# Kernel tuning notes

Hardware: AMD Instinct MI355X
Metric: run time of the kernel (lower is better)

## Reference

```python
import jax, jax.numpy as jnp
import numpy as np

B, C, H, W, NH = 8, 512, 32, 32, 8
HD = C // NH
SCALE = HD ** -0.5


def reshape_for_attention(t, num_heads):
    # faithful to torch: view(B,nh,hd,HW) -> permute(0,3,1,2) -> view(B*nh, HW, hd)
    b, c, h, w = t.shape
    t = t.reshape(b, num_heads, c // num_heads, h * w)
    t = jnp.transpose(t, (0, 3, 1, 2))  # [B, HW, nh, hd]
    return t.reshape(b * num_heads, h * w, c // num_heads)


def reshape_from_attention(t, original_shape, num_heads):
    b, c, h, w = original_shape
    t = t.reshape(b, h * w, num_heads, c // num_heads)
    t = jnp.transpose(t, (0, 2, 3, 1))  # [B, nh, hd, HW]
    return t.reshape(b, c, h, w)


def setup_inputs() -> dict:
    key = jax.random.key(0)
    ks = jax.random.split(key, 6)
    s = (2.0 / C) ** 0.5  # kaiming-ish scale for 1x1 convs
    return {
        "x": jax.random.normal(ks[0], (B, C, H, W), dtype=jnp.float32),
        "wq": jax.random.normal(ks[1], (C, C), dtype=jnp.float32) * s,
        "wk": jax.random.normal(ks[2], (C, C), dtype=jnp.float32) * s,
        "wv": jax.random.normal(ks[3], (C, C), dtype=jnp.float32) * s,
        "wo": jax.random.normal(ks[4], (C, C), dtype=jnp.float32) * s,
        "ln_gamma": jnp.ones((C,), dtype=jnp.float32),
        "ln_beta": jnp.zeros((C,), dtype=jnp.float32),
        "gamma": jnp.zeros((1,), dtype=jnp.float32),
    }


def reference(x, wq, wk, wv, wo, ln_gamma, ln_beta, gamma):
    b, c, h, w = x.shape
    residual = x
    # 1x1 convs, no bias == channel GEMMs
    q = jnp.einsum('oc,bchw->bohw', wq, x)
    k = jnp.einsum('oc,bchw->bohw', wk, x)
    v = jnp.einsum('oc,bchw->bohw', wv, x)
    q = reshape_for_attention(q, NH)  # [B*nh, N, hd]
    k = reshape_for_attention(k, NH)
    v = reshape_for_attention(v, NH)
    attn = jnp.einsum('bnd,bmd->bnm', q, k) * SCALE  # [B*nh, N, N]
    attn = jax.nn.softmax(attn, axis=-1)
    attn_out = jnp.einsum('bnm,bmd->bnd', attn, v)
    attn_out = reshape_from_attention(attn_out, (b, c, h, w), NH)
    out = jnp.einsum('oc,bchw->bohw', wo, attn_out)
    # post-LN over channel dim
    out = jnp.transpose(out, (0, 2, 3, 1))  # [B,H,W,C]
    mu = jnp.mean(out, axis=-1, keepdims=True)
    var = jnp.var(out, axis=-1, keepdims=True)
    out = (out - mu) * jax.lax.rsqrt(var + 1e-5) * ln_gamma + ln_beta
    out = jnp.transpose(out, (0, 3, 1, 2))  # [B,C,H,W]
    return gamma * out + residual
```

## Files before the change

kernel.cpp:

```cpp
#include <hip/hip_runtime.h>
#include <hip/hip_bf16.h>


#define B_  8
#define C_  512
#define N_  1024
#define NH_ 8
#define HD_ 64

typedef __bf16 bf16x8 __attribute__((ext_vector_type(8)));
typedef __bf16 bf16x4 __attribute__((ext_vector_type(4)));
typedef float  f32x4  __attribute__((ext_vector_type(4)));

#define MFMA16(a, b, c) __builtin_amdgcn_mfma_f32_16x16x32_bf16((a), (b), (c), 0, 0, 0)

__device__ __forceinline__ void gload16(const void* g, void* l) {
    __builtin_amdgcn_global_load_lds(
        (const __attribute__((address_space(1))) unsigned int*)g,
        (__attribute__((address_space(3))) unsigned int*)l, 16, 0, 0);
}

__global__ __launch_bounds__(256) void k_prep(const float* __restrict__ x,
                                              const float* __restrict__ wq,
                                              const float* __restrict__ wk,
                                              const float* __restrict__ wv,
                                              const float* __restrict__ wo,
                                              __bf16* __restrict__ xt,
                                              __bf16* __restrict__ wcat) {
    __shared__ float tile[64][68];
    int blk = blockIdx.x;
    int tid = threadIdx.x;
    if (blk < 1024) {
        int b   = blk >> 7;
        int rem = blk & 127;
        int ct  = rem >> 4;
        int pt  = rem & 15;
        int c0 = ct * 64, p0 = pt * 64;
        for (int i = 0; i < 4; ++i) {
            int vi = i * 256 + tid;
            int c = vi >> 4, p4 = (vi & 15) * 4;
            f32x4 v = *(const f32x4*)(x + ((size_t)(b * C_ + c0 + c)) * N_ + p0 + p4);
            *(f32x4*)&tile[c][p4] = v;
        }
        __syncthreads();
        for (int i = 0; i < 4; ++i) {
            int vi = i * 256 + tid;
            int p = vi >> 4, c4 = (vi & 15) * 4;
            bf16x4 v;
            for (int j = 0; j < 4; ++j) v[j] = (__bf16)tile[c4 + j][p];
            *(bf16x4*)(xt + ((size_t)(b * N_ + p0 + p)) * C_ + c0 + c4) = v;
        }
    } else {
        int idx = (blk - 1024) * 256 + tid;
        int mat = idx >> 16;
        int off = (idx & 65535) * 4;
        const float* w = (mat == 0) ? wq : (mat == 1) ? wk : (mat == 2) ? wv : wo;
        f32x4 v = *(const f32x4*)(w + off);
        bf16x4 o;
        for (int j = 0; j < 4; ++j) o[j] = (__bf16)v[j];
        *(bf16x4*)(wcat + (size_t)mat * 262144 + off) = o;
    }
}

__global__ __launch_bounds__(256) void k_qkv(const __bf16* __restrict__ xt,
                                             const __bf16* __restrict__ wcat,
                                             __bf16* __restrict__ qa,
                                             __bf16* __restrict__ ka,
                                             __bf16* __restrict__ vt) {
    int blk  = blockIdx.x;
    int mat  = blk >> 8;
    int rem  = blk & 255;
    int b    = rem >> 5;
    int tile = rem & 31;
    int tid = threadIdx.x, lane = tid & 63, wid = tid >> 6;
    int quad = lane >> 4, l16 = lane & 15;

    const __bf16* w = wcat + (size_t)mat * 262144;
    const __bf16 *A, *Bm;
    int am0, bn0;
    if (mat < 2) {
        int mt = tile >> 2, nt = tile & 3;
        A   = xt + (size_t)b * N_ * C_;  am0 = mt * 128 + (wid >> 1) * 64;
        Bm  = w;                         bn0 = nt * 128 + (wid & 1) * 64;
    } else {
        int mt = tile & 3, nt = tile >> 2;
        A   = w;                         am0 = mt * 128 + (wid >> 1) * 64;
        Bm  = xt + (size_t)b * N_ * C_;  bn0 = nt * 128 + (wid & 1) * 64;
    }

    f32x4 acc[4][4] = {};
    for (int ks = 0; ks < 16; ++ks) {
        int kc = ks * 32 + quad * 8;
        bf16x8 af[4], bfr[4];
        for (int i = 0; i < 4; ++i)
            af[i] = *(const bf16x8*)(A + (size_t)(am0 + i * 16 + l16) * C_ + kc);
        for (int i = 0; i < 4; ++i)
            bfr[i] = *(const bf16x8*)(Bm + (size_t)(bn0 + i * 16 + l16) * C_ + kc);
        for (int mi = 0; mi < 4; ++mi)
            for (int ni = 0; ni < 4; ++ni)
                acc[mi][ni] = MFMA16(af[mi], bfr[ni], acc[mi][ni]);
    }

    if (mat < 2) {
        __bf16* dst = (mat == 0) ? qa : ka;
        for (int mi = 0; mi < 4; ++mi)
            for (int r = 0; r < 4; ++r) {
                int p = am0 + mi * 16 + quad * 4 + r;
                int g = b * NH_ + (p >> 7);
                int nbase = (p & 127) * 8;
                for (int ni = 0; ni < 4; ++ni) {
                    int o = bn0 + ni * 16 + l16;
                    dst[((size_t)g * N_ + nbase + (o >> 6)) * HD_ + (o & 63)] =
                        (__bf16)acc[mi][ni][r];
                }
            }
    } else {
        for (int mi = 0; mi < 4; ++mi)
            for (int r = 0; r < 4; ++r) {
                int o = am0 + mi * 16 + quad * 4 + r;
                int m = o & 63, i = o >> 6;
                for (int ni = 0; ni < 4; ++ni) {
                    int p = bn0 + ni * 16 + l16;
                    int g = b * NH_ + (p >> 7);
                    vt[((size_t)g * HD_ + m) * N_ + (p & 127) * 8 + i] =
                        (__bf16)acc[mi][ni][r];
                }
            }
    }
}

__global__ __launch_bounds__(256) void k_attn(const __bf16* __restrict__ qa,
                                              const __bf16* __restrict__ ka,
                                              const __bf16* __restrict__ vt,
                                              __bf16* __restrict__ ap) {
    __shared__ __bf16 Kb[2][4096];
    __shared__ __bf16 Vb[2][4096];
    __shared__ __bf16 plds[4][32][64];
    int blk = blockIdx.x;
    int g  = ((blk & 7) << 3) | ((blk >> 3) & 7);
    int qb = blk >> 6;
    int tid = threadIdx.x, lane = tid & 63, wid = tid >> 6;
    int quad = lane >> 4, l16 = lane & 15;
    int q0 = qb * 128 + wid * 32;

    const __bf16* qp = qa + (size_t)g * N_ * HD_;
    const char* kbb = (const char*)(ka + (size_t)g * N_ * HD_);
    const char* vbb = (const char*)(vt + (size_t)g * HD_ * N_);

    bf16x8 qA0 = *(const bf16x8*)(qp + (size_t)(q0 + l16) * HD_ + quad * 8);
    bf16x8 qA1 = *(const bf16x8*)(qp + (size_t)(q0 + l16) * HD_ + 32 + quad * 8);
    bf16x8 qB0 = *(const bf16x8*)(qp + (size_t)(q0 + 16 + l16) * HD_ + quad * 8);
    bf16x8 qB1 = *(const bf16x8*)(qp + (size_t)(q0 + 16 + l16) * HD_ + 32 + quad * 8);

    int lrow = lane >> 3;
    int scol = ((lane & 7) * 16) ^ (lrow << 4);
    const char* kSrc = kbb + (size_t)(wid * 16 + lrow) * 128  + scol;
    const char* vSrc = vbb + (size_t)(wid * 16 + lrow) * 2048 + scol;
    char* kds[2] = {(char*)&Kb[0][0] + wid * 2048, (char*)&Kb[1][0] + wid * 2048};
    char* vds[2] = {(char*)&Vb[0][0] + wid * 2048, (char*)&Vb[1][0] + wid * 2048};

    gload16(kSrc,          kds[0]);
    gload16(kSrc + 1024,   kds[0] + 1024);
    gload16(vSrc,          vds[0]);
    gload16(vSrc + 16384,  vds[0] + 1024);
    asm volatile("s_waitcnt vmcnt(0)" ::: "memory");
    __syncthreads();

    float liA = 0.f, liB = 0.f;
    f32x4 oA[4] = {}, oB[4] = {};
    const float sc = 0.125f * 1.44269504088896340736f;
    const int swzP = (l16 & 7) * 8;
    const int fsw  = (l16 & 7) << 4;

    int cur = 0;
    for (int t = 0; t < 16; ++t) {
        int jn = ((t + 1) & 15) * 64;
        gload16(kSrc + (size_t)jn * 128,          kds[cur ^ 1]);
        gload16(kSrc + (size_t)jn * 128 + 1024,   kds[cur ^ 1] + 1024);
        gload16(vSrc + jn * 2,                    vds[cur ^ 1]);
        gload16(vSrc + jn * 2 + 16384,            vds[cur ^ 1] + 1024);

        const char* kt = (const char*)&Kb[cur][0] - (size_t)0;
        kt = (const char*)&Kb[cur][0];
        bf16x8 kc0[4], kc1[4];
        for (int tt = 0; tt < 4; ++tt) {
            int rb = (tt * 16 + l16) * 128;
            kc0[tt] = *(const bf16x8*)(kt + rb + ((quad * 16) ^ fsw));
            kc1[tt] = *(const bf16x8*)(kt + rb + ((64 + quad * 16) ^ fsw));
        }
        f32x4 sA[4] = {}, sB[4] = {};
        for (int tt = 0; tt < 4; ++tt) {
            sA[tt] = MFMA16(kc0[tt], qA0, sA[tt]);
            sA[tt] = MFMA16(kc1[tt], qA1, sA[tt]);
            sB[tt] = MFMA16(kc0[tt], qB0, sB[tt]);
            sB[tt] = MFMA16(kc1[tt], qB1, sB[tt]);
        }

        for (int tt = 0; tt < 4; ++tt) {
            bf16x4 pkA, pkB;
            for (int r = 0; r < 4; ++r) {
                float pvA = exp2f(sA[tt][r] * sc);
                float pvB = exp2f(sB[tt][r] * sc);
                liA += pvA; liB += pvB;
                pkA[r] = (__bf16)pvA; pkB[r] = (__bf16)pvB;
            }
            int ks = (tt * 16 + quad * 4) ^ swzP;
            *(bf16x4*)&plds[wid][l16][ks]      = pkA;
            *(bf16x4*)&plds[wid][16 + l16][ks] = pkB;
        }

        asm volatile("" ::: "memory");
        const char* vtl = (const char*)&Vb[cur][0];
        for (int h = 0; h < 2; ++h) {
            int ks = (h * 32 + quad * 8) ^ swzP;
            bf16x8 pA = *(const bf16x8*)&plds[wid][l16][ks];
            bf16x8 pB = *(const bf16x8*)&plds[wid][16 + l16][ks];
            for (int dd = 0; dd < 4; ++dd) {
                bf16x8 av = *(const bf16x8*)(vtl + (dd * 16 + l16) * 128
                                             + ((h * 64 + quad * 16) ^ fsw));
                oA[dd] = MFMA16(av, pA, oA[dd]);
                oB[dd] = MFMA16(av, pB, oB[dd]);
            }
        }
        asm volatile("" ::: "memory");

        asm volatile("s_waitcnt vmcnt(0)" ::: "memory");
        __syncthreads();
        cur ^= 1;
    }

    liA += __shfl_xor(liA, 16, 64); liA += __shfl_xor(liA, 32, 64);
    liB += __shfl_xor(liB, 16, 64); liB += __shfl_xor(liB, 32, 64);

    int b = g >> 3, hi = g & 7;
    float invA = 1.0f / liA, invB = 1.0f / liB;
    int nA = q0 + l16, nB = q0 + 16 + l16;
    __bf16* dA = ap + ((size_t)(b * N_ + hi * 128 + (nA >> 3))) * C_ + (nA & 7) * 64;
    __bf16* dB = ap + ((size_t)(b * N_ + hi * 128 + (nB >> 3))) * C_ + (nB & 7) * 64;
    for (int dd = 0; dd < 4; ++dd) {
        bf16x4 oa, ob;
        for (int r = 0; r < 4; ++r) {
            oa[r] = (__bf16)(oA[dd][r] * invA);
            ob[r] = (__bf16)(oB[dd][r] * invB);
        }
        *(bf16x4*)(dA + dd * 16 + quad * 4) = oa;
        *(bf16x4*)(dB + dd * 16 + quad * 4) = ob;
    }
}

__global__ __launch_bounds__(256) void k_oproj(const __bf16* __restrict__ apm,
                                               const __bf16* __restrict__ wob,
                                               __bf16* __restrict__ o0) {
    int blk = blockIdx.x;
    int b = blk >> 5, tile = blk & 31;
    int mt = tile >> 2, nt = tile & 3;
    int tid = threadIdx.x, lane = tid & 63, wid = tid >> 6;
    int quad = lane >> 4, l16 = lane & 15;
    int am0 = mt * 128 + (wid >> 1) * 64;
    int bn0 = nt * 128 + (wid & 1) * 64;
    const __bf16* A = apm + (size_t)b * N_ * C_;

    f32x4 acc[4][4] = {};
    for (int ks = 0; ks < 16; ++ks) {
        int kc = ks * 32 + quad * 8;
        bf16x8 af[4], bfr[4];
        for (int i = 0; i < 4; ++i)
            af[i] = *(const bf16x8*)(A + (size_t)(am0 + i * 16 + l16) * C_ + kc);
        for (int i = 0; i < 4; ++i)
            bfr[i] = *(const bf16x8*)(wob + (size_t)(bn0 + i * 16 + l16) * C_ + kc);
        for (int mi = 0; mi < 4; ++mi)
            for (int ni = 0; ni < 4; ++ni)
                acc[mi][ni] = MFMA16(af[mi], bfr[ni], acc[mi][ni]);
    }
    for (int mi = 0; mi < 4; ++mi)
        for (int r = 0; r < 4; ++r) {
            int p = am0 + mi * 16 + quad * 4 + r;
            __bf16* dst = o0 + ((size_t)(b * N_ + p)) * C_;
            for (int ni = 0; ni < 4; ++ni)
                dst[bn0 + ni * 16 + l16] = (__bf16)acc[mi][ni][r];
        }
}

__global__ __launch_bounds__(256) void k_ln(const __bf16* __restrict__ o0,
                                            const float* __restrict__ x,
                                            const float* __restrict__ lng,
                                            const float* __restrict__ lnb,
                                            const float* __restrict__ gm,
                                            float* __restrict__ out) {
    __shared__ __bf16 tile[32][C_ + 4];
    int blk = blockIdx.x;
    int b = blk >> 5, pt = blk & 31;
    int p0 = pt * 32;
    int tid = threadIdx.x, lane = tid & 63, wid = tid >> 6;
    float g = gm[0];
    float lg[8], lb[8];
    *(f32x4*)&lg[0] = *(const f32x4*)(lng + lane * 8);
    *(f32x4*)&lg[4] = *(const f32x4*)(lng + lane * 8 + 4);
    *(f32x4*)&lb[0] = *(const f32x4*)(lnb + lane * 8);
    *(f32x4*)&lb[4] = *(const f32x4*)(lnb + lane * 8 + 4);

    for (int i = 0; i < 8; ++i) {
        int p = wid * 8 + i;
        bf16x8 v = *(const bf16x8*)(o0 + ((size_t)(b * N_ + p0 + p)) * C_ + lane * 8);
        float f[8], s = 0.f, ss = 0.f;
        for (int j = 0; j < 8; ++j) { f[j] = (float)v[j]; s += f[j]; ss += f[j] * f[j]; }
        for (int d = 1; d < 64; d <<= 1) { s += __shfl_xor(s, d, 64); ss += __shfl_xor(ss, d, 64); }
        float mean = s * (1.f / 512.f);
        float var  = ss * (1.f / 512.f) - mean * mean;
        float rstd = rsqrtf(fmaxf(var, 0.f) + 1e-5f);
        bf16x4 o1, o2;
        for (int j = 0; j < 4; ++j)
            o1[j] = (__bf16)(g * ((f[j] - mean) * rstd * lg[j] + lb[j]));
        for (int j = 0; j < 4; ++j)
            o2[j] = (__bf16)(g * ((f[j + 4] - mean) * rstd * lg[j + 4] + lb[j + 4]));
        __bf16* dst = &tile[p][lane * 8];
        *(bf16x4*)dst = o1;
        *(bf16x4*)(dst + 4) = o2;
    }
    __syncthreads();
    for (int it = 0; it < 16; ++it) {
        int task = it * 256 + tid;
        int c = task >> 3, p4 = (task & 7) * 4;
        f32x4 xr = *(const f32x4*)(x + ((size_t)(b * C_ + c)) * N_ + p0 + p4);
        f32x4 o;
        for (int j = 0; j < 4; ++j)
            o[j] = (float)tile[p4 + j][c] + xr[j];
        *(f32x4*)(out + ((size_t)(b * C_ + c)) * N_ + p0 + p4) = o;
    }
}

__global__ void k_qkv8f(const float* __restrict__ x, const float* __restrict__ wq,
                        const float* __restrict__ wk, const float* __restrict__ wv,
                        float* __restrict__ qa, float* __restrict__ ka,
                        float* __restrict__ va, int g0) {
    int idx = blockIdx.x * 256 + threadIdx.x;
    int m = idx & 63, n = (idx >> 6) & 1023, Gl = (idx >> 16) & 1, mat = idx >> 17;
    int G = g0 + Gl, b = G >> 3, hb = G & 7;
    int p = hb * 128 + (n >> 3), o = (n & 7) * 64 + m;
    const float* w = (mat == 0) ? wq : (mat == 1) ? wk : wv;
    float acc = 0.f;
    for (int c = 0; c < C_; ++c)
        acc += w[(size_t)o * C_ + c] * x[((size_t)b * C_ + c) * N_ + p];
    float* dst = (mat == 0) ? qa : (mat == 1) ? ka : va;
    dst[((size_t)Gl * N_ + n) * HD_ + m] = acc;
}
__global__ void k_attn8f(const float* __restrict__ qa, const float* __restrict__ ka,
                         const float* __restrict__ va, float* __restrict__ ac, int g0) {
    int idx = blockIdx.x * 256 + threadIdx.x;
    int i = idx & 1023, Gl = (idx >> 10) & 1, G = g0 + Gl;
    const float* qrow = qa + ((size_t)Gl * N_ + i) * HD_;
    float q[HD_];
    for (int m = 0; m < HD_; ++m) q[m] = qrow[m];
    const float* kb = ka + (size_t)Gl * N_ * HD_;
    const float* vb = va + (size_t)Gl * N_ * HD_;
    float mx = -1e30f;
    for (int j = 0; j < N_; ++j) {
        float s = 0.f;
        for (int m = 0; m < HD_; ++m) s += q[m] * kb[j * HD_ + m];
        mx = fmaxf(mx, s);
    }
    mx *= 0.125f;
    float l = 0.f, ov[HD_];
    for (int m = 0; m < HD_; ++m) ov[m] = 0.f;
    for (int j = 0; j < N_; ++j) {
        float s = 0.f;
        for (int m = 0; m < HD_; ++m) s += q[m] * kb[j * HD_ + m];
        float pj = __expf(s * 0.125f - mx);
        l += pj;
        for (int m = 0; m < HD_; ++m) ov[m] += pj * vb[j * HD_ + m];
    }
    float inv = 1.0f / l;
    int b = G >> 3, hb = G & 7;
    int p = hb * 128 + (i >> 3), cb = (i & 7) * 64;
    for (int m = 0; m < HD_; ++m)
        ac[((size_t)b * C_ + cb + m) * N_ + p] = ov[m] * inv;
}
__global__ void k_oln8f(float* __restrict__ ac, const float* __restrict__ wo,
                        const float* __restrict__ x, const float* __restrict__ lng,
                        const float* __restrict__ lnb, const float* __restrict__ gm) {
    int tid = threadIdx.x, lane = tid & 63, wid = tid >> 6;
    int bp = blockIdx.x * 4 + wid;
    int b = bp >> 10, p = bp & 1023;
    float oc[8];
    for (int h = 0; h < 8; ++h) oc[h] = 0.f;
    for (int c = 0; c < C_; ++c) {
        float cv = ac[((size_t)b * C_ + c) * N_ + p];
        for (int h = 0; h < 8; ++h)
            oc[h] += wo[(size_t)(h * 64 + lane) * C_ + c] * cv;
    }
    float s = 0.f, ss = 0.f;
    for (int h = 0; h < 8; ++h) { s += oc[h]; ss += oc[h] * oc[h]; }
    for (int d = 1; d < 64; d <<= 1) { s += __shfl_xor(s, d, 64); ss += __shfl_xor(ss, d, 64); }
    float mean = s * (1.f / 512.f);
    float var  = ss * (1.f / 512.f) - mean * mean;
    float rstd = rsqrtf(fmaxf(var, 0.f) + 1e-5f);
    float g = gm[0];
    for (int h = 0; h < 8; ++h) {
        int o = h * 64 + lane;
        float xv = x[((size_t)b * C_ + o) * N_ + p];
        ac[((size_t)b * C_ + o) * N_ + p] =
            g * ((oc[h] - mean) * rstd * lng[o] + lnb[o]) + xv;
    }
}

extern "C" void kernel_launch(void* const* d_in, const int* in_sizes, int n_in,
                              void* d_out, int out_size, void* d_ws, size_t ws_size,
                              hipStream_t stream) {
    const float* x   = (const float*)d_in[0];
    const float* wq  = (const float*)d_in[1];
    const float* wk  = (const float*)d_in[2];
    const float* wv  = (const float*)d_in[3];
    const float* wo  = (const float*)d_in[4];
    const float* lng = (const float*)d_in[5];
    const float* lnb = (const float*)d_in[6];
    const float* gm  = (const float*)d_in[7];
    float* out = (float*)d_out;
    char* wsb = (char*)d_ws;

    if (ws_size >= ((size_t)18 << 20)) {
        __bf16* xt   = (__bf16*)wsb;
        __bf16* wcat = (__bf16*)(wsb + ((size_t)8 << 20));
        __bf16* Qa   = (__bf16*)(wsb + ((size_t)10 << 20));
        __bf16* Ka   = (__bf16*)d_out;
        __bf16* VaT  = (__bf16*)((char*)d_out + ((size_t)8 << 20));
        __bf16* ap   = xt;
        __bf16* o0   = Qa;
        __bf16* wob  = wcat + 3 * 262144;

        k_prep  <<<2048, 256, 0, stream>>>(x, wq, wk, wv, wo, xt, wcat);
        k_qkv   <<<768,  256, 0, stream>>>(xt, wcat, Qa, Ka, VaT);
        k_attn  <<<512,  256, 0, stream>>>(Qa, Ka, VaT, ap);
        k_oproj <<<256,  256, 0, stream>>>(ap, wob, o0);
        k_ln    <<<256,  256, 0, stream>>>(o0, x, lng, lnb, gm, out);
    } else {
        float* qa = (float*)(wsb + 256);
        float* ka = qa + 2 * N_ * HD_;
        float* va = ka + 2 * N_ * HD_;
        for (int g0 = 0; g0 < 64; g0 += 2) {
            k_qkv8f <<<1536, 256, 0, stream>>>(x, wq, wk, wv, qa, ka, va, g0);
            k_attn8f<<<8,    256, 0, stream>>>(qa, ka, va, out, g0);
        }
        k_oln8f<<<2048, 256, 0, stream>>>(out, wo, x, lng, lnb, gm);
    }
}
```

Baseline: 201.1 us.

## Stage QKV and output-projection GEMM tiles through double-buffered swizzled LDS

The QKV and output-projection GEMM kernels now load 128x32 A and B tiles into shared memory with direct global-to-LDS loads and double buffering, instead of each wave reading its operand fragments straight from global memory. The tiles are shared by the four waves, which cuts redundant global and L2 traffic, and the next K-slice is prefetched while MFMAs run on the current one. An XOR swizzle is meant to avoid LDS bank conflicts. The cost is 32 KB of LDS per block and a barrier on every K step.

```diff
diff --git a/kernel.cpp b/kernel.cpp
--- a/kernel.cpp
+++ b/kernel.cpp
@@ -67,6 +67,8 @@
                                              __bf16* __restrict__ qa,
                                              __bf16* __restrict__ ka,
                                              __bf16* __restrict__ vt) {
+    __shared__ __bf16 As[2][4096];
+    __shared__ __bf16 Bs[2][4096];
     int blk  = blockIdx.x;
     int mat  = blk >> 8;
     int rem  = blk & 255;
@@ -80,36 +82,62 @@
     int am0, bn0;
     if (mat < 2) {
         int mt = tile >> 2, nt = tile & 3;
-        A   = xt + (size_t)b * N_ * C_;  am0 = mt * 128 + (wid >> 1) * 64;
-        Bm  = w;                         bn0 = nt * 128 + (wid & 1) * 64;
+        A   = xt + (size_t)b * N_ * C_;  am0 = mt * 128;
+        Bm  = w;                         bn0 = nt * 128;
     } else {
         int mt = tile & 3, nt = tile >> 2;
-        A   = w;                         am0 = mt * 128 + (wid >> 1) * 64;
-        Bm  = xt + (size_t)b * N_ * C_;  bn0 = nt * 128 + (wid & 1) * 64;
-    }
+        A   = w;                         am0 = mt * 128;
+        Bm  = xt + (size_t)b * N_ * C_;  bn0 = nt * 128;
+    }
+    int wr = (wid >> 1) * 64, wc = (wid & 1) * 64;
+
+    int lrow = wid * 16 + (lane >> 2);
+    int scol = ((lane & 3) * 16) ^ ((lrow & 3) << 4);
+    const char* aS0 = (const char*)A  + (size_t)(am0 + lrow) * 1024 + scol;
+    const char* aS1 = aS0 + 65536;
+    const char* bS0 = (const char*)Bm + (size_t)(bn0 + lrow) * 1024 + scol;
+    const char* bS1 = bS0 + 65536;
+    char* aD[2] = {(char*)&As[0][0] + wid * 1024, (char*)&As[1][0] + wid * 1024};
+    char* bD[2] = {(char*)&Bs[0][0] + wid * 1024, (char*)&Bs[1][0] + wid * 1024};
+
+    gload16(aS0, aD[0]);  gload16(aS1, aD[0] + 4096);
+    gload16(bS0, bD[0]);  gload16(bS1, bD[0] + 4096);
+    asm volatile("s_waitcnt vmcnt(0)" ::: "memory");
+    __syncthreads();
 
     f32x4 acc[4][4] = {};
-    for (int ks = 0; ks < 16; ++ks) {
-        int kc = ks * 32 + quad * 8;
+    const int fo = (quad * 16) ^ ((l16 & 3) << 4);
+    int cur = 0;
+    for (int t = 0; t < 16; ++t) {
+        int kb = ((t + 1) & 15) * 64;
+        gload16(aS0 + kb, aD[cur ^ 1]);  gload16(aS1 + kb, aD[cur ^ 1] + 4096);
+        gload16(bS0 + kb, bD[cur ^ 1]);  gload16(bS1 + kb, bD[cur ^ 1] + 4096);
+
+        const char* at = (const char*)&As[cur][0];
+        const char* bt = (const char*)&Bs[cur][0];
         bf16x8 af[4], bfr[4];
         for (int i = 0; i < 4; ++i)
-            af[i] = *(const bf16x8*)(A + (size_t)(am0 + i * 16 + l16) * C_ + kc);
+            af[i]  = *(const bf16x8*)(at + (wr + i * 16 + l16) * 64 + fo);
         for (int i = 0; i < 4; ++i)
-            bfr[i] = *(const bf16x8*)(Bm + (size_t)(bn0 + i * 16 + l16) * C_ + kc);
+            bfr[i] = *(const bf16x8*)(bt + (wc + i * 16 + l16) * 64 + fo);
         for (int mi = 0; mi < 4; ++mi)
             for (int ni = 0; ni < 4; ++ni)
                 acc[mi][ni] = MFMA16(af[mi], bfr[ni], acc[mi][ni]);
+
+        asm volatile("s_waitcnt vmcnt(0)" ::: "memory");
+        __syncthreads();
+        cur ^= 1;
     }
 
     if (mat < 2) {
         __bf16* dst = (mat == 0) ? qa : ka;
         for (int mi = 0; mi < 4; ++mi)
             for (int r = 0; r < 4; ++r) {
-                int p = am0 + mi * 16 + quad * 4 + r;
+                int p = am0 + wr + mi * 16 + quad * 4 + r;
                 int g = b * NH_ + (p >> 7);
                 int nbase = (p & 127) * 8;
                 for (int ni = 0; ni < 4; ++ni) {
-                    int o = bn0 + ni * 16 + l16;
+                    int o = bn0 + wc + ni * 16 + l16;
                     dst[((size_t)g * N_ + nbase + (o >> 6)) * HD_ + (o & 63)] =
                         (__bf16)acc[mi][ni][r];
                 }
@@ -117,10 +145,10 @@
     } else {
         for (int mi = 0; mi < 4; ++mi)
             for (int r = 0; r < 4; ++r) {
-                int o = am0 + mi * 16 + quad * 4 + r;
+                int o = am0 + wr + mi * 16 + quad * 4 + r;
                 int m = o & 63, i = o >> 6;
                 for (int ni = 0; ni < 4; ++ni) {
-                    int p = bn0 + ni * 16 + l16;
+                    int p = bn0 + wc + ni * 16 + l16;
                     int g = b * NH_ + (p >> 7);
                     vt[((size_t)g * HD_ + m) * N_ + (p & 127) * 8 + i] =
                         (__bf16)acc[mi][ni][r];
@@ -180,8 +208,7 @@
         gload16(vSrc + jn * 2,                    vds[cur ^ 1]);
         gload16(vSrc + jn * 2 + 16384,            vds[cur ^ 1] + 1024);
 
-        const char* kt = (const char*)&Kb[cur][0] - (size_t)0;
-        kt = (const char*)&Kb[cur][0];
+        const char* kt = (const char*)&Kb[cur][0];
         bf16x8 kc0[4], kc1[4];
         for (int tt = 0; tt < 4; ++tt) {
             int rb = (tt * 16 + l16) * 128;
@@ -251,33 +278,60 @@
 __global__ __launch_bounds__(256) void k_oproj(const __bf16* __restrict__ apm,
                                                const __bf16* __restrict__ wob,
                                                __bf16* __restrict__ o0) {
+    __shared__ __bf16 As[2][4096];
+    __shared__ __bf16 Bs[2][4096];
     int blk = blockIdx.x;
     int b = blk >> 5, tile = blk & 31;
     int mt = tile >> 2, nt = tile & 3;
     int tid = threadIdx.x, lane = tid & 63, wid = tid >> 6;
     int quad = lane >> 4, l16 = lane & 15;
-    int am0 = mt * 128 + (wid >> 1) * 64;
-    int bn0 = nt * 128 + (wid & 1) * 64;
+    int am0 = mt * 128, bn0 = nt * 128;
+    int wr = (wid >> 1) * 64, wc = (wid & 1) * 64;
     const __bf16* A = apm + (size_t)b * N_ * C_;
 
+    int lrow = wid * 16 + (lane >> 2);
+    int scol = ((lane & 3) * 16) ^ ((lrow & 3) << 4);
+    const char* aS0 = (const char*)A   + (size_t)(am0 + lrow) * 1024 + scol;
+    const char* aS1 = aS0 + 65536;
+    const char* bS0 = (const char*)wob + (size_t)(bn0 + lrow) * 1024 + scol;
+    const char* bS1 = bS0 + 65536;
+    char* aD[2] = {(char*)&As[0][0] + wid * 1024, (char*)&As[1][0] + wid * 1024};
+    char* bD[2] = {(char*)&Bs[0][0] + wid * 1024, (char*)&Bs[1][0] + wid * 1024};
+
+    gload16(aS0, aD[0]);  gload16(aS1, aD[0] + 4096);
+    gload16(bS0, bD[0]);  gload16(bS1, bD[0] + 4096);
+    asm volatile("s_waitcnt vmcnt(0)" ::: "memory");
+    __syncthreads();
+
     f32x4 acc[4][4] = {};
-    for (int ks = 0; ks < 16; ++ks) {
-        int kc = ks * 32 + quad * 8;
+    const int fo = (quad * 16) ^ ((l16 & 3) << 4);
+    int cur = 0;
+    for (int t = 0; t < 16; ++t) {
+        int kb = ((t + 1) & 15) * 64;
+        gload16(aS0 + kb, aD[cur ^ 1]);  gload16(aS1 + kb, aD[cur ^ 1] + 4096);
+        gload16(bS0 + kb, bD[cur ^ 1]);  gload16(bS1 + kb, bD[cur ^ 1] + 4096);
+
+        const char* at = (const char*)&As[cur][0];
+        const char* bt = (const char*)&Bs[cur][0];
         bf16x8 af[4], bfr[4];
         for (int i = 0; i < 4; ++i)
-            af[i] = *(const bf16x8*)(A + (size_t)(am0 + i * 16 + l16) * C_ + kc);
+            af[i]  = *(const bf16x8*)(at + (wr + i * 16 + l16) * 64 + fo);
         for (int i = 0; i < 4; ++i)
-            bfr[i] = *(const bf16x8*)(wob + (size_t)(bn0 + i * 16 + l16) * C_ + kc);
+            bfr[i] = *(const bf16x8*)(bt + (wc + i * 16 + l16) * 64 + fo);
         for (int mi = 0; mi < 4; ++mi)
             for (int ni = 0; ni < 4; ++ni)
                 acc[mi][ni] = MFMA16(af[mi], bfr[ni], acc[mi][ni]);
+
+        asm volatile("s_waitcnt vmcnt(0)" ::: "memory");
+        __syncthreads();
+        cur ^= 1;
     }
     for (int mi = 0; mi < 4; ++mi)
         for (int r = 0; r < 4; ++r) {
-            int p = am0 + mi * 16 + quad * 4 + r;
+            int p = am0 + wr + mi * 16 + quad * 4 + r;
             __bf16* dst = o0 + ((size_t)(b * N_ + p)) * C_;
             for (int ni = 0; ni < 4; ++ni)
-                dst[bn0 + ni * 16 + l16] = (__bf16)acc[mi][ni][r];
+                dst[bn0 + wc + ni * 16 + l16] = (__bf16)acc[mi][ni][r];
         }
 }
 
```

Result: faster. 166.4 us (-17.3%).
